# Performance work log

Measured on AMD Instinct MI355X. Metric: run time of the kernel, lower is better.

## Reference

```python
import jax, jax.numpy as jnp
import numpy as np

B, N0, N1, N2 = 8, 4096, 1024, 256
G, AF = 1024, 32


def knn_interp(xf, px, py, k):
    # xf: [B,Nx,C] features at source points px [B,Nx,3]; interpolate onto py [B,Ny,3]
    d2 = jnp.sum((py[:, :, None, :] - px[:, None, :, :]) ** 2, axis=-1)  # [B,Ny,Nx]
    neg_d2, idx = jax.lax.top_k(-d2, k)                                   # [B,Ny,k]
    w = 1.0 / jnp.maximum(-neg_d2, 1e-16)                                 # inverse squared distance
    feats = jnp.take_along_axis(xf[:, None, :, :], idx[..., None], axis=2)  # [B,Ny,k,C]
    return jnp.sum(feats * w[..., None], axis=2) / jnp.sum(w, axis=2)[..., None]


def _lin(x, w, b):
    return x @ w + b


def _forward(pos0, x1, pos1, x2, pos2, x3, pos3, approach_point,
             fp3_w1, fp3_b1, fp3_w2, fp3_b2,
             fp2_w1, fp2_b1, fp2_w2, fp2_b2,
             fp1_w1, fp1_b1, fp1_w2, fp1_b2, fp1_w3, fp1_b3,
             enc_w1, enc_b1, enc_w2, enc_b2,
             head_w1, head_b1, head_w2, head_b2, head_w3, head_b3):
    # fp3: global feature (1 pt) -> sa2 points, k=1
    h = knn_interp(x3, pos3, pos2, 1)
    h = jnp.concatenate([h, x2], axis=-1)           # [B,N2,G+256]
    h = jax.nn.relu(_lin(h, fp3_w1, fp3_b1))
    h = _lin(h, fp3_w2, fp3_b2)                     # [B,N2,256]
    # fp2: sa2 -> sa1, k=3
    h = knn_interp(h, pos2, pos1, 3)
    h = jnp.concatenate([h, x1], axis=-1)           # [B,N1,384]
    h = jax.nn.relu(_lin(h, fp2_w1, fp2_b1))
    h = _lin(h, fp2_w2, fp2_b2)                     # [B,N1,128]
    # fp1: sa1 -> sa0, k=3; x_skip at sa0 is raw xyz
    h = knn_interp(h, pos1, pos0, 3)
    h = jnp.concatenate([h, pos0], axis=-1)         # [B,N0,131]
    h = jax.nn.relu(_lin(h, fp1_w1, fp1_b1))
    h = jax.nn.relu(_lin(h, fp1_w2, fp1_b2))
    h = _lin(h, fp1_w3, fp1_b3)                     # [B,N0,128]
    # approach point encoder + broadcast per cloud (batch_idx gather)
    af = _lin(jax.nn.relu(_lin(approach_point, enc_w1, enc_b1)), enc_w2, enc_b2)  # [B,AF]
    af = jnp.broadcast_to(af[:, None, :], (h.shape[0], h.shape[1], af.shape[-1]))
    h = jnp.concatenate([h, af], axis=-1)           # [B,N0,128+AF]
    # head MLP (dropout is identity in eval)
    h = jax.nn.relu(_lin(h, head_w1, head_b1))
    h = jax.nn.relu(_lin(h, head_w2, head_b2))
    return _lin(h, head_w3, head_b3)                # [B,N0,1]


def setup_inputs() -> dict:
    key = jax.random.key(0)
    ks = jax.random.split(key, 24)
    rn = lambda k_, shp, s=1.0: jax.random.normal(k_, shp, dtype=jnp.float32) * s
    S = 0.02
    inp = {
        'pos0': rn(ks[0], (B, N0, 3)),
        'x1': rn(ks[1], (B, N1, 128)),
        'pos1': rn(ks[2], (B, N1, 3)),
        'x2': rn(ks[3], (B, N2, 256)),
        'pos2': rn(ks[4], (B, N2, 3)),
        'x3': rn(ks[5], (B, 1, G)),
        'pos3': rn(ks[6], (B, 1, 3)),
        'approach_point': rn(ks[7], (B, 3)),
        'fp3_w1': rn(ks[8], (G + 256, 256), S), 'fp3_b1': jnp.zeros((256,), jnp.float32),
        'fp3_w2': rn(ks[9], (256, 256), S), 'fp3_b2': jnp.zeros((256,), jnp.float32),
        'fp2_w1': rn(ks[10], (256 + 128, 256), S), 'fp2_b1': jnp.zeros((256,), jnp.float32),
        'fp2_w2': rn(ks[11], (256, 128), S), 'fp2_b2': jnp.zeros((128,), jnp.float32),
        'fp1_w1': rn(ks[12], (128 + 3, 128), S), 'fp1_b1': jnp.zeros((128,), jnp.float32),
        'fp1_w2': rn(ks[13], (128, 128), S), 'fp1_b2': jnp.zeros((128,), jnp.float32),
        'fp1_w3': rn(ks[14], (128, 128), S), 'fp1_b3': jnp.zeros((128,), jnp.float32),
        'enc_w1': rn(ks[15], (3, 32), S), 'enc_b1': jnp.zeros((32,), jnp.float32),
        'enc_w2': rn(ks[16], (32, AF), S), 'enc_b2': jnp.zeros((AF,), jnp.float32),
        'head_w1': rn(ks[17], (128 + AF, 128), S), 'head_b1': jnp.zeros((128,), jnp.float32),
        'head_w2': rn(ks[18], (128, 128), S), 'head_b2': jnp.zeros((128,), jnp.float32),
        'head_w3': rn(ks[19], (128, 1), S), 'head_b3': jnp.zeros((1,), jnp.float32),
    }
    return inp


def reference(pos0, x1, pos1, x2, pos2, x3, pos3, approach_point,
              fp3_w1, fp3_b1, fp3_w2, fp3_b2,
              fp2_w1, fp2_b1, fp2_w2, fp2_b2,
              fp1_w1, fp1_b1, fp1_w2, fp1_b2, fp1_w3, fp1_b3,
              enc_w1, enc_b1, enc_w2, enc_b2,
              head_w1, head_b1, head_w2, head_b2, head_w3, head_b3):
    return _forward(pos0, x1, pos1, x2, pos2, x3, pos3, approach_point,
                    fp3_w1, fp3_b1, fp3_w2, fp3_b2,
                    fp2_w1, fp2_b1, fp2_w2, fp2_b2,
                    fp1_w1, fp1_b1, fp1_w2, fp1_b2, fp1_w3, fp1_b3,
                    enc_w1, enc_b1, enc_w2, enc_b2,
                    head_w1, head_b1, head_w2, head_b2, head_w3, head_b3)
```

## Files before the change

kernel.cpp:

```cpp
#include <hip/hip_runtime.h>

#define BB   8
#define N0   4096
#define N1   1024
#define N2   256
#define GG   1024
#define AFW  32

typedef unsigned long long u64;
typedef double d4 __attribute__((ext_vector_type(4)));

__device__ __forceinline__ void ins3(u64 key, u64& k0, u64& k1, u64& k2) {
  const bool c0 = key < k0, c1 = key < k1, c2 = key < k2;
  const u64 n2 = c1 ? k1 : (c2 ? key : k2);
  const u64 n1 = c0 ? k0 : (c1 ? key : k1);
  k0 = c0 ? key : k0; k1 = n1; k2 = n2;
}

template <int NCAND, int QTOT>
__device__ __forceinline__ void
knn_body(int idx, const float* __restrict__ cpos, const float* __restrict__ qpos,
         int* __restrict__ idxo, double* __restrict__ wno,
         double* __restrict__ ps, u64* __restrict__ topw) {
  const int qc = idx % (QTOT / 64);
  const int b = idx / (QTOT / 64);
  const int tid = threadIdx.x;
  {
    const float* src = cpos + (size_t)b * NCAND * 3;
    for (int i = tid; i < NCAND * 3; i += 256) ps[i] = (double)src[i];
  }
  __syncthreads();

  const int wave = tid >> 6, lane = tid & 63;
  const size_t gq = (size_t)b * QTOT + qc * 64 + lane;
  const double qx = (double)qpos[gq * 3 + 0];
  const double qy = (double)qpos[gq * 3 + 1];
  const double qz = (double)qpos[gq * 3 + 2];

  constexpr int NC4 = NCAND / 4;
  u64 k0 = ~0ull, k1 = ~0ull, k2 = ~0ull;
  const int kbeg = wave * NC4;
#pragma unroll 2
  for (int kk = 0; kk < NC4; ++kk) {
    const int k = kbeg + kk;
    const double dx = qx - ps[3 * k + 0];
    const double dy = qy - ps[3 * k + 1];
    const double dz = qz - ps[3 * k + 2];
    const double d = dx * dx + dy * dy + dz * dz;
    const u64 key = (((u64)__double_as_longlong(d)) & ~1023ull) | (unsigned)k;
    ins3(key, k0, k1, k2);
  }
  topw[(wave * 64 + lane) * 3 + 0] = k0;
  topw[(wave * 64 + lane) * 3 + 1] = k1;
  topw[(wave * 64 + lane) * 3 + 2] = k2;
  __syncthreads();

  if (tid < 64) {
    u64 m0 = ~0ull, m1 = ~0ull, m2 = ~0ull;
#pragma unroll
    for (int w = 0; w < 4; ++w)
#pragma unroll
      for (int s = 0; s < 3; ++s)
        ins3(topw[(w * 64 + tid) * 3 + s], m0, m1, m2);
    const double d0 = __longlong_as_double((long long)(m0 & ~1023ull));
    const double d1 = __longlong_as_double((long long)(m1 & ~1023ull));
    const double d2 = __longlong_as_double((long long)(m2 & ~1023ull));
    const double w0 = 1.0 / fmax(d0, 1e-16);
    const double w1 = 1.0 / fmax(d1, 1e-16);
    const double w2 = 1.0 / fmax(d2, 1e-16);
    const double inv = 1.0 / (w0 + w1 + w2);
    const size_t go = (size_t)b * QTOT + qc * 64 + tid;
    idxo[go * 3 + 0] = (int)(m0 & 1023ull);
    idxo[go * 3 + 1] = (int)(m1 & 1023ull);
    idxo[go * 3 + 2] = (int)(m2 & 1023ull);
    wno[go * 3 + 0] = w0 * inv;
    wno[go * 3 + 1] = w1 * inv;
    wno[go * 3 + 2] = w2 * inv;
  }
}

__global__ void __launch_bounds__(256)
k_setup(const float* __restrict__ pos0, const float* __restrict__ pos1,
        const float* __restrict__ pos2,
        const float* __restrict__ x3, const float* __restrict__ w1,
        double* __restrict__ y3p,
        const float* __restrict__ ap,
        const float* __restrict__ ew1, const float* __restrict__ eb1,
        const float* __restrict__ ew2, const float* __restrict__ eb2,
        float* __restrict__ af,
        int* __restrict__ idx2, double* __restrict__ wn2,
        int* __restrict__ idx1, double* __restrict__ wn1,
        int* __restrict__ mtab) {
  __shared__ double ps[3072];
  __shared__ u64 topw[768];
  __shared__ double hs[32];
  const int bi = blockIdx.x;
  const int tid = threadIdx.x;

  if (bi == 0) {
    if (tid < 64) {
      const int m = tid & 15, g = tid >> 4;
      const d4 z = {0.0, 0.0, 0.0, 0.0};
      const double e = (g == 0) ? (double)(m + 1) : 0.0;
      d4 r1 = __builtin_amdgcn_mfma_f64_16x16x4f64(e, 1.0, z, 0, 0, 0);
      d4 r2 = __builtin_amdgcn_mfma_f64_16x16x4f64(1.0, e, z, 0, 0, 0);
#pragma unroll
      for (int r = 0; r < 4; ++r) {
        const int row = ((int)r1[r] - 1) & 15;
        const int col = ((int)r2[r] - 1) & 15;
        mtab[tid * 4 + r] = (row << 8) | col;
      }
    }
  } else if (bi < 33) {
    const int idx = bi - 1;
    const int b = idx & 7, part = idx >> 3;
    double acc = 0.0;
    const float* xr = x3 + (size_t)b * GG + part * 256;
    const float* wr = w1 + (size_t)part * 256 * 256;
    for (int k = 0; k < 256; ++k)
      acc += (double)xr[k] * (double)wr[k * 256 + tid];
    y3p[((size_t)b * 4 + part) * 256 + tid] = acc;

    if (part == 0) {
      if (tid < 32) {
        double a = (double)eb1[tid];
        for (int k = 0; k < 3; ++k)
          a += (double)ap[b * 3 + k] * (double)ew1[k * 32 + tid];
        hs[tid] = fmax(a, 0.0);
      }
      __syncthreads();
      if (tid < 32) {
        double a = (double)eb2[tid];
        for (int k = 0; k < 32; ++k)
          a += hs[k] * (double)ew2[k * 32 + tid];
        af[b * 32 + tid] = (float)a;
      }
    }
  } else if (bi < 161) {
    knn_body<N2, N1>(bi - 33, pos2, pos1, idx2, wn2, ps, topw);
  } else {
    knn_body<N1, N0>(bi - 161, pos1, pos0, idx1, wn1, ps, topw);
  }
}

template <int NT, int K, int JW, int INS_S, int OUTS_S, bool RELU, bool Y3>
__device__ __forceinline__ void
mfma_tile(const float* __restrict__ inL, float* __restrict__ outP,
          const float* __restrict__ w, const float* __restrict__ bias,
          const double* __restrict__ y3b, int lane, int jb, int rb, int4 rc4) {
  const int m = lane & 15, g = lane >> 4;
  int rw[4], cl[4];
  rw[0] = (rc4.x >> 8) & 15; cl[0] = rc4.x & 15;
  rw[1] = (rc4.y >> 8) & 15; cl[1] = rc4.y & 15;
  rw[2] = (rc4.z >> 8) & 15; cl[2] = rc4.z & 15;
  rw[3] = (rc4.w >> 8) & 15; cl[3] = rc4.w & 15;
  d4 acc[NT];
#pragma unroll
  for (int t = 0; t < NT; ++t) {
#pragma unroll
    for (int r = 0; r < 4; ++r) {
      const int j = jb + t * 16 + cl[r];
      double base = (double)bias[j];
      if (Y3) base += y3b[j] + y3b[256 + j] + y3b[512 + j] + y3b[768 + j];
      acc[t][r] = base;
    }
  }
  constexpr int FULL = K / 4;
#pragma unroll 2
  for (int s = 0; s < FULL; ++s) {
    const double a = (double)inL[(rb + m) * INS_S + 4 * s + g];
    const float* wr = w + (size_t)(4 * s + g) * JW + jb + m;
#pragma unroll
    for (int t = 0; t < NT; ++t) {
      const double bv = (double)wr[t * 16];
      acc[t] = __builtin_amdgcn_mfma_f64_16x16x4f64(a, bv, acc[t], 0, 0, 0);
    }
  }
  if constexpr ((K & 3) != 0) {
    const int kk = FULL * 4 + g;
    const double a = (double)inL[(rb + m) * INS_S + kk];
    const bool ok = kk < K;
    const float* wr = w + (size_t)kk * JW + jb + m;
#pragma unroll
    for (int t = 0; t < NT; ++t) {
      double bv = 0.0;
      if (ok) bv = (double)wr[t * 16];
      acc[t] = __builtin_amdgcn_mfma_f64_16x16x4f64(a, bv, acc[t], 0, 0, 0);
    }
  }
#pragma unroll
  for (int t = 0; t < NT; ++t)
#pragma unroll
    for (int r = 0; r < 4; ++r) {
      float v = (float)acc[t][r];
      if (RELU) v = fmaxf(v, 0.f);
      outP[(size_t)(rb + rw[r]) * OUTS_S + jb + t * 16 + cl[r]] = v;
    }
}

__global__ void __launch_bounds__(512)
k_fp3(const float* __restrict__ x2, const double* __restrict__ y3p,
      const float* __restrict__ w1, const float* __restrict__ b1,
      const float* __restrict__ w2, const float* __restrict__ b2,
      float* __restrict__ h2, const int* __restrict__ mtab) {
  __shared__ float rows[16 * 261];
  __shared__ float t[16 * 261];
  const int b = blockIdx.x >> 4;
  const int p0 = (blockIdx.x & 15) * 16;
  const int tid = threadIdx.x;
  const int lane = tid & 63, wv = tid >> 6;
  const int4 rc4 = *(const int4*)(mtab + lane * 4);
  {
    const int c = tid & 255, ph = tid >> 8;
    for (int i = 0; i < 8; ++i) {
      const int p = i * 2 + ph;
      rows[p * 261 + c] = x2[((size_t)b * N2 + p0 + p) * 256 + c];
    }
  }
  __syncthreads();
  mfma_tile<2, 256, 256, 261, 261, true, true>(rows, t, w1 + (size_t)1024 * 256,
                                               b1, y3p + (size_t)b * 1024,
                                               lane, wv * 32, 0, rc4);
  __syncthreads();
  mfma_tile<2, 256, 256, 261, 256, false, false>(t, h2 + ((size_t)b * N2 + p0) * 256,
                                                 w2, b2, nullptr, lane, wv * 32, 0, rc4);
}

__global__ void __launch_bounds__(512)
k_fp2(const float* __restrict__ h2, const float* __restrict__ x1,
      const int* __restrict__ idx2, const double* __restrict__ wn2,
      const float* __restrict__ w1, const float* __restrict__ b1,
      const float* __restrict__ w2, const float* __restrict__ b2,
      float* __restrict__ h1, const int* __restrict__ mtab) {
  __shared__ float rows[16 * 389];
  __shared__ float t[16 * 261];
  __shared__ int sidx[16][3];
  __shared__ double swn[16][3];
  const int b = blockIdx.x >> 6;
  const int p0 = (blockIdx.x & 63) * 16;
  const int tid = threadIdx.x;
  const int lane = tid & 63, wv = tid >> 6;
  const int4 rc4 = *(const int4*)(mtab + lane * 4);

  if (tid < 48) {
    const int p = tid / 3, i = tid % 3;
    const size_t g = ((size_t)b * N1 + p0 + p) * 3 + i;
    sidx[p][i] = idx2[g];
    swn[p][i] = wn2[g];
  }
  __syncthreads();

  {
    const float* base = h2 + (size_t)b * N2 * 256;
    const int c = tid & 255, ph = tid >> 8;
    for (int i = 0; i < 8; ++i) {
      const int p = i * 2 + ph;
      const double v = swn[p][0] * (double)base[(size_t)sidx[p][0] * 256 + c] +
                       swn[p][1] * (double)base[(size_t)sidx[p][1] * 256 + c] +
                       swn[p][2] * (double)base[(size_t)sidx[p][2] * 256 + c];
      rows[p * 389 + c] = (float)v;
    }
    const int c2 = tid & 127, p4 = tid >> 7;
    for (int i = 0; i < 4; ++i) {
      const int p = i * 4 + p4;
      rows[p * 389 + 256 + c2] = x1[((size_t)b * N1 + p0 + p) * 128 + c2];
    }
  }
  __syncthreads();
  mfma_tile<2, 384, 256, 389, 261, true, false>(rows, t, w1, b1, nullptr,
                                                lane, wv * 32, 0, rc4);
  __syncthreads();
  mfma_tile<1, 256, 128, 261, 128, false, false>(t, h1 + ((size_t)b * N1 + p0) * 128,
                                                 w2, b2, nullptr, lane, wv * 16, 0, rc4);
}

__global__ void __launch_bounds__(512)
k_fp1head(const float* __restrict__ h1, const float* __restrict__ pos0,
          const int* __restrict__ idx1, const double* __restrict__ wn1,
          const float* __restrict__ afv,
          const float* __restrict__ w1, const float* __restrict__ b1,
          const float* __restrict__ w2, const float* __restrict__ b2,
          const float* __restrict__ w3, const float* __restrict__ b3,
          const float* __restrict__ hw1, const float* __restrict__ hb1,
          const float* __restrict__ hw2, const float* __restrict__ hb2,
          const float* __restrict__ hw3, const float* __restrict__ hb3,
          float* __restrict__ out, const int* __restrict__ mtab) {
  __shared__ float A[32 * 137];
  __shared__ float Bf[32 * 165];
  __shared__ int sidx[32][3];
  __shared__ double swn[32][3];
  const int b = blockIdx.x >> 7;
  const int p0 = (blockIdx.x & 127) * 32;
  const int tid = threadIdx.x;
  const int lane = tid & 63, wv = tid >> 6;
  const int rb = (wv >> 2) * 16;
  const int jb = (wv & 3) * 32;
  const int4 rc4 = *(const int4*)(mtab + lane * 4);

  if (tid < 96) {
    const int p = tid / 3, i = tid % 3;
    const size_t g = ((size_t)b * N0 + p0 + p) * 3 + i;
    sidx[p][i] = idx1[g];
    swn[p][i] = wn1[g];
  }
  if (tid >= 96 && tid < 128) {
    const int p = tid - 96;
    for (int c = 131; c < 137; ++c) A[p * 137 + c] = 0.f;
  }
  for (int x = tid; x < 32 * 32; x += 512)
    Bf[(x >> 5) * 165 + 128 + (x & 31)] = afv[b * 32 + (x & 31)];
  __syncthreads();

  {
    const int c = tid & 127, pq = tid >> 7;
    const float* basep = h1 + (size_t)b * N1 * 128;
    for (int i = 0; i < 8; ++i) {
      const int p = i * 4 + pq;
      const double v = swn[p][0] * (double)basep[(size_t)sidx[p][0] * 128 + c] +
                       swn[p][1] * (double)basep[(size_t)sidx[p][1] * 128 + c] +
                       swn[p][2] * (double)basep[(size_t)sidx[p][2] * 128 + c];
      A[p * 137 + c] = (float)v;
    }
  }
  if (tid < 96) {
    const int p = tid / 3, i = tid % 3;
    A[p * 137 + 128 + i] = pos0[((size_t)b * N0 + p0 + p) * 3 + i];
  }
  __syncthreads();

  mfma_tile<2, 131, 128, 137, 165, true,  false>(A,  Bf, w1,  b1,  nullptr, lane, jb, rb, rc4);
  __syncthreads();
  mfma_tile<2, 128, 128, 165, 137, true,  false>(Bf, A,  w2,  b2,  nullptr, lane, jb, rb, rc4);
  __syncthreads();
  mfma_tile<2, 128, 128, 137, 165, false, false>(A,  Bf, w3,  b3,  nullptr, lane, jb, rb, rc4);
  __syncthreads();
  mfma_tile<2, 160, 128, 165, 137, true,  false>(Bf, A,  hw1, hb1, nullptr, lane, jb, rb, rc4);
  __syncthreads();
  mfma_tile<2, 128, 128, 137, 165, true,  false>(A,  Bf, hw2, hb2, nullptr, lane, jb, rb, rc4);
  __syncthreads();

  {
    const int p = tid >> 4, l = tid & 15;
    double acc = 0.0;
    for (int k = l; k < 128; k += 16)
      acc += (double)Bf[p * 165 + k] * (double)hw3[k];
    for (int off = 8; off > 0; off >>= 1)
      acc += __shfl_down(acc, off, 16);
    if (l == 0)
      out[(size_t)b * N0 + p0 + p] = (float)(acc + (double)hb3[0]);
  }
}

extern "C" void kernel_launch(void* const* d_in, const int* in_sizes, int n_in,
                              void* d_out, int out_size, void* d_ws, size_t ws_size,
                              hipStream_t stream) {
  const float* pos0 = (const float*)d_in[0];
  const float* x1   = (const float*)d_in[1];
  const float* pos1 = (const float*)d_in[2];
  const float* x2   = (const float*)d_in[3];
  const float* pos2 = (const float*)d_in[4];
  const float* x3   = (const float*)d_in[5];
  const float* ap   = (const float*)d_in[7];
  const float* fp3w1 = (const float*)d_in[8];
  const float* fp3b1 = (const float*)d_in[9];
  const float* fp3w2 = (const float*)d_in[10];
  const float* fp3b2 = (const float*)d_in[11];
  const float* fp2w1 = (const float*)d_in[12];
  const float* fp2b1 = (const float*)d_in[13];
  const float* fp2w2 = (const float*)d_in[14];
  const float* fp2b2 = (const float*)d_in[15];
  const float* fp1w1 = (const float*)d_in[16];
  const float* fp1b1 = (const float*)d_in[17];
  const float* fp1w2 = (const float*)d_in[18];
  const float* fp1b2 = (const float*)d_in[19];
  const float* fp1w3 = (const float*)d_in[20];
  const float* fp1b3 = (const float*)d_in[21];
  const float* encw1 = (const float*)d_in[22];
  const float* encb1 = (const float*)d_in[23];
  const float* encw2 = (const float*)d_in[24];
  const float* encb2 = (const float*)d_in[25];
  const float* hw1 = (const float*)d_in[26];
  const float* hb1 = (const float*)d_in[27];
  const float* hw2 = (const float*)d_in[28];
  const float* hb2 = (const float*)d_in[29];
  const float* hw3 = (const float*)d_in[30];
  const float* hb3 = (const float*)d_in[31];
  float* out = (float*)d_out;

  char* p = (char*)d_ws;
  double* y3p = (double*)p; p += (size_t)BB * 4 * 256 * 8;
  double* wn2 = (double*)p; p += (size_t)BB * N1 * 3 * 8;
  double* wn1 = (double*)p; p += (size_t)BB * N0 * 3 * 8;
  float*  af  = (float*)p;  p += (size_t)BB * 32 * 4;
  int*    idx2= (int*)p;    p += (size_t)BB * N1 * 3 * 4;
  int*    idx1= (int*)p;    p += (size_t)BB * N0 * 3 * 4;
  float*  h2  = (float*)p;  p += (size_t)BB * N2 * 256 * 4;
  float*  h1  = (float*)p;  p += (size_t)BB * N1 * 128 * 4;
  int*    mtab= (int*)p;    p += 1024;

  hipLaunchKernelGGL(k_setup, dim3(673), dim3(256), 0, stream,
                     pos0, pos1, pos2, x3, fp3w1, y3p,
                     ap, encw1, encb1, encw2, encb2, af,
                     idx2, wn2, idx1, wn1, mtab);
  hipLaunchKernelGGL(k_fp3, dim3(BB * N2 / 16), dim3(512), 0, stream,
                     x2, y3p, fp3w1, fp3b1, fp3w2, fp3b2, h2, mtab);
  hipLaunchKernelGGL(k_fp2, dim3(BB * N1 / 16), dim3(512), 0, stream,
                     h2, x1, idx2, wn2, fp2w1, fp2b1, fp2w2, fp2b2, h1, mtab);
  hipLaunchKernelGGL(k_fp1head, dim3(BB * N0 / 32), dim3(512), 0, stream,
                     h1, pos0, idx1, wn1, af,
                     fp1w1, fp1b1, fp1w2, fp1b2, fp1w3, fp1b3,
                     hw1, hb1, hw2, hb2, hw3, hb3, out, mtab);
}
```

Baseline: 328.3 us.

## Split fp3 into two kernels over output halves and software-pipeline weight loads

The fp3 stage is split into two kernels, each launched with 256 blocks of 256 threads, and each block computes half of the output columns. This doubles the number of blocks from 128 to 256 so more of the GPU's compute units get work. The intermediate activation goes through a global scratch buffer that reuses the h1 region, which adds an extra kernel launch and a global round-trip. Separately, the shared MFMA tile loop now prefetches the next two k-steps of weights into registers ahead of use, to hide global load latency, at the cost of more register pressure.

```diff
diff --git a/kernel.cpp b/kernel.cpp
--- a/kernel.cpp
+++ b/kernel.cpp
@@ -166,14 +166,34 @@
     }
   }
   constexpr int FULL = K / 4;
-#pragma unroll 2
-  for (int s = 0; s < FULL; ++s) {
-    const double a = (double)inL[(rb + m) * INS_S + 4 * s + g];
-    const float* wr = w + (size_t)(4 * s + g) * JW + jb + m;
-#pragma unroll
-    for (int t = 0; t < NT; ++t) {
-      const double bv = (double)wr[t * 16];
-      acc[t] = __builtin_amdgcn_mfma_f64_16x16x4f64(a, bv, acc[t], 0, 0, 0);
+  const float* wbase = w + (size_t)g * JW + jb + m;
+  double b0[NT], b1[NT];
+#pragma unroll
+  for (int t = 0; t < NT; ++t) {
+    b0[t] = (double)wbase[t * 16];
+    b1[t] = (double)wbase[(size_t)4 * JW + t * 16];
+  }
+  for (int s = 0; s < FULL; s += 2) {
+    double n0[NT], n1[NT];
+    const bool more = (s + 2) < FULL;
+    if (more) {
+#pragma unroll
+      for (int t = 0; t < NT; ++t) {
+        n0[t] = (double)wbase[(size_t)(4 * (s + 2)) * JW + t * 16];
+        n1[t] = (double)wbase[(size_t)(4 * (s + 3)) * JW + t * 16];
+      }
+    }
+    const double a0 = (double)inL[(rb + m) * INS_S + 4 * s + g];
+#pragma unroll
+    for (int t = 0; t < NT; ++t)
+      acc[t] = __builtin_amdgcn_mfma_f64_16x16x4f64(a0, b0[t], acc[t], 0, 0, 0);
+    const double a1 = (double)inL[(rb + m) * INS_S + 4 * (s + 1) + g];
+#pragma unroll
+    for (int t = 0; t < NT; ++t)
+      acc[t] = __builtin_amdgcn_mfma_f64_16x16x4f64(a1, b1[t], acc[t], 0, 0, 0);
+    if (more) {
+#pragma unroll
+      for (int t = 0; t < NT; ++t) { b0[t] = n0[t]; b1[t] = n1[t]; }
     }
   }
   if constexpr ((K & 3) != 0) {
@@ -198,32 +218,44 @@
     }
 }
 
-__global__ void __launch_bounds__(512)
-k_fp3(const float* __restrict__ x2, const double* __restrict__ y3p,
-      const float* __restrict__ w1, const float* __restrict__ b1,
-      const float* __restrict__ w2, const float* __restrict__ b2,
-      float* __restrict__ h2, const int* __restrict__ mtab) {
+__global__ void __launch_bounds__(256)
+k_fp3a(const float* __restrict__ x2, const double* __restrict__ y3p,
+       const float* __restrict__ w1, const float* __restrict__ b1,
+       float* __restrict__ t3, const int* __restrict__ mtab) {
   __shared__ float rows[16 * 261];
-  __shared__ float t[16 * 261];
-  const int b = blockIdx.x >> 4;
-  const int p0 = (blockIdx.x & 15) * 16;
+  const int jh = blockIdx.x & 1;
+  const int pg = blockIdx.x >> 1;
+  const int b = pg >> 4;
+  const int p0 = (pg & 15) * 16;
   const int tid = threadIdx.x;
   const int lane = tid & 63, wv = tid >> 6;
   const int4 rc4 = *(const int4*)(mtab + lane * 4);
-  {
-    const int c = tid & 255, ph = tid >> 8;
-    for (int i = 0; i < 8; ++i) {
-      const int p = i * 2 + ph;
-      rows[p * 261 + c] = x2[((size_t)b * N2 + p0 + p) * 256 + c];
-    }
-  }
-  __syncthreads();
-  mfma_tile<2, 256, 256, 261, 261, true, true>(rows, t, w1 + (size_t)1024 * 256,
-                                               b1, y3p + (size_t)b * 1024,
-                                               lane, wv * 32, 0, rc4);
-  __syncthreads();
-  mfma_tile<2, 256, 256, 261, 256, false, false>(t, h2 + ((size_t)b * N2 + p0) * 256,
-                                                 w2, b2, nullptr, lane, wv * 32, 0, rc4);
+  for (int p = 0; p < 16; ++p)
+    rows[p * 261 + tid] = x2[((size_t)b * N2 + p0 + p) * 256 + tid];
+  __syncthreads();
+  mfma_tile<2, 256, 256, 261, 256, true, true>(
+      rows, t3 + ((size_t)b * N2 + p0) * 256, w1 + (size_t)1024 * 256, b1,
+      y3p + (size_t)b * 1024, lane, jh * 128 + wv * 32, 0, rc4);
+}
+
+__global__ void __launch_bounds__(256)
+k_fp3b(const float* __restrict__ t3,
+       const float* __restrict__ w2, const float* __restrict__ b2,
+       float* __restrict__ h2, const int* __restrict__ mtab) {
+  __shared__ float rows[16 * 261];
+  const int jh = blockIdx.x & 1;
+  const int pg = blockIdx.x >> 1;
+  const int b = pg >> 4;
+  const int p0 = (pg & 15) * 16;
+  const int tid = threadIdx.x;
+  const int lane = tid & 63, wv = tid >> 6;
+  const int4 rc4 = *(const int4*)(mtab + lane * 4);
+  for (int p = 0; p < 16; ++p)
+    rows[p * 261 + tid] = t3[((size_t)b * N2 + p0 + p) * 256 + tid];
+  __syncthreads();
+  mfma_tile<2, 256, 256, 261, 256, false, false>(
+      rows, h2 + ((size_t)b * N2 + p0) * 256, w2, b2, nullptr,
+      lane, jh * 128 + wv * 32, 0, rc4);
 }
 
 __global__ void __launch_bounds__(512)
@@ -397,13 +429,16 @@
   float*  h2  = (float*)p;  p += (size_t)BB * N2 * 256 * 4;
   float*  h1  = (float*)p;  p += (size_t)BB * N1 * 128 * 4;
   int*    mtab= (int*)p;    p += 1024;
+  float*  t3  = h1;
 
   hipLaunchKernelGGL(k_setup, dim3(673), dim3(256), 0, stream,
                      pos0, pos1, pos2, x3, fp3w1, y3p,
                      ap, encw1, encb1, encw2, encb2, af,
                      idx2, wn2, idx1, wn1, mtab);
-  hipLaunchKernelGGL(k_fp3, dim3(BB * N2 / 16), dim3(512), 0, stream,
-                     x2, y3p, fp3w1, fp3b1, fp3w2, fp3b2, h2, mtab);
+  hipLaunchKernelGGL(k_fp3a, dim3(256), dim3(256), 0, stream,
+                     x2, y3p, fp3w1, fp3b1, t3, mtab);
+  hipLaunchKernelGGL(k_fp3b, dim3(256), dim3(256), 0, stream,
+                     t3, fp3w2, fp3b2, h2, mtab);
   hipLaunchKernelGGL(k_fp2, dim3(BB * N1 / 16), dim3(512), 0, stream,
                      h2, x1, idx2, wn2, fp2w1, fp2b1, fp2w2, fp2b2, h1, mtab);
   hipLaunchKernelGGL(k_fp1head, dim3(BB * N0 / 32), dim3(512), 0, stream,
```

New measurement: 313.7 us. 4.4% less time.
